# Kernel tuning notes

Hardware: AMD Instinct MI355X
Metric: run time of the kernel (lower is better)

The kernel has to match this reference:

```python
import jax, jax.numpy as jnp
import numpy as np

S, B, H, NH = 2048, 1, 4096, 32
HD = H // NH            # 128
ROT = int(HD * 0.25)    # 32 partial rotary dims
BASE = 10000.0


def setup_inputs() -> dict:
    key = jax.random.key(0)
    ks = jax.random.split(key, 4)
    hidden_states = jax.random.normal(ks[0], (S, B, H), dtype=jnp.float32)
    W_qkv = jax.random.normal(ks[1], (3 * H, H), dtype=jnp.float32) * 0.02
    b_qkv = jnp.zeros((3 * H,), dtype=jnp.float32)
    W_dense = jax.random.normal(ks[2], (H, H), dtype=jnp.float32) * 0.02
    b_dense = jnp.zeros((H,), dtype=jnp.float32)
    # causal left-to-right mask, True = attend
    attention_mask = jnp.tril(jnp.ones((S, S), dtype=bool))[None, None]  # [1,1,S,S]
    return dict(hidden_states=hidden_states, attention_mask=attention_mask,
                W_qkv=W_qkv, b_qkv=b_qkv, W_dense=W_dense, b_dense=b_dense)


def _rotate_half(x):
    x1, x2 = jnp.split(x, 2, axis=-1)
    return jnp.concatenate((-x2, x1), axis=-1)


def reference(hidden_states, attention_mask, W_qkv, b_qkv, W_dense, b_dense):
    S_, B_ = hidden_states.shape[:2]
    qkv = hidden_states @ W_qkv.T + b_qkv                    # [S,B,3H]
    qkv = qkv.reshape(S_, B_, NH, 3 * HD)
    q, k, v = qkv[..., :HD], qkv[..., HD:2 * HD], qkv[..., 2 * HD:]

    # partial rotary embedding (GPT-NeoX style, offset=0, no KV cache)
    inv_freq = 1.0 / (BASE ** (jnp.arange(0, ROT, 2, dtype=jnp.float32) / ROT))
    t = jnp.arange(S_, dtype=jnp.float32)
    freqs = jnp.einsum('s,d->sd', t, inv_freq)               # [S,ROT/2]
    emb = jnp.concatenate((freqs, freqs), axis=-1)           # [S,ROT]
    cos = jnp.cos(emb)[:, None, None, :]                     # [S,1,1,ROT]
    sin = jnp.sin(emb)[:, None, None, :]

    def rope(x):
        return x * cos + _rotate_half(x) * sin

    q = jnp.concatenate((rope(q[..., :ROT]), q[..., ROT:]), axis=-1)
    k = jnp.concatenate((rope(k[..., :ROT]), k[..., ROT:]), axis=-1)

    # scaled dot-product attention with explicit score matrix
    scores = jnp.einsum('sbhd,tbhd->bhst', q, k) / np.float32(np.sqrt(HD))
    scores = jnp.where(attention_mask, scores, jnp.float32(-10000.0))
    probs = jax.nn.softmax(scores, axis=-1)                  # [B,NH,S,S]
    ctx = jnp.einsum('bhst,tbhd->sbhd', probs, v).reshape(S_, B_, H)
    return ctx @ W_dense.T + b_dense                         # [S,B,H]
```

## Files before the change

### kernel.cpp

```cpp
#include <hip/hip_runtime.h>
#include <hip/hip_bf16.h>
#include <math.h>

typedef __bf16 bf16_t;
typedef bf16_t bf16x8 __attribute__((ext_vector_type(8)));
typedef bf16_t bf16x4 __attribute__((ext_vector_type(4)));
typedef float floatx4 __attribute__((ext_vector_type(4)));

#define S_LEN 2048
#define QK_LD 8192

__global__ void convert_all(const float* __restrict__ a, bf16_t* __restrict__ ao,
                            const float* __restrict__ b, bf16_t* __restrict__ bo,
                            const float* __restrict__ c, bf16_t* __restrict__ co) {
    int i = blockIdx.x * 256 + threadIdx.x;
    const float* src; bf16_t* dst; int j;
    if (i < 2097152)        { src = a; dst = ao; j = i; }
    else if (i < 14680064)  { src = b; dst = bo; j = i - 2097152; }
    else                    { src = c; dst = co; j = i - 14680064; }
    float4 v = ((const float4*)src)[j];
    bf16x4 o;
    o.x = (bf16_t)v.x; o.y = (bf16_t)v.y; o.z = (bf16_t)v.z; o.w = (bf16_t)v.w;
    ((bf16x4*)dst)[j] = o;
}

__device__ __forceinline__ void async_copy16(const void* g, void* l) {
    __builtin_amdgcn_global_load_lds(
        (const __attribute__((address_space(1))) unsigned int*)g,
        (__attribute__((address_space(3))) unsigned int*)l, 16, 0, 0);
}

__device__ __forceinline__ void fast_sincos(float x, float* sn, float* cs) {
    float rev = x * 0.15915494309189535f;
    rev = rev - floorf(rev);
    *sn = __builtin_amdgcn_sinf(rev);
    *cs = __builtin_amdgcn_cosf(rev);
}

__global__ __launch_bounds__(256) void qkv_gemm(
    const bf16_t* __restrict__ A, const bf16_t* __restrict__ B,
    const float* __restrict__ bias, bf16_t* __restrict__ qkout,
    bf16_t* __restrict__ vt)
{
    __shared__ bf16_t As[128 * 32];
    __shared__ bf16_t Bs[128 * 32];
    const int K = 4096;
    const int t    = threadIdx.x;
    const int lane = t & 63;
    const int w    = t >> 6;
    const int l15  = lane & 15;
    const int quad = lane >> 4;
    const int bm = blockIdx.y, bn = blockIdx.x;
    const int mw = (w >> 1) * 64, nw = (w & 1) * 64;

    floatx4 acc[4][4];
    #pragma unroll
    for (int i = 0; i < 4; i++)
        #pragma unroll
        for (int j = 0; j < 4; j++)
            acc[i][j] = (floatx4){0.f, 0.f, 0.f, 0.f};

    const int r0 = t >> 2;
    const int c0 = (t & 3) * 8;
    const bf16_t* Aptr = A + (size_t)(bm * 128 + r0) * K + c0;
    const bf16_t* Bptr = B + (size_t)(bn * 128 + r0) * K + c0;
    bf16_t* AsW = As + t * 8;
    bf16_t* BsW = Bs + t * 8;

    for (int k0 = 0; k0 < K; k0 += 32) {
        __syncthreads();
        async_copy16(Aptr + k0, AsW);
        async_copy16(Aptr + k0 + (size_t)64 * K, AsW + 2048);
        async_copy16(Bptr + k0, BsW);
        async_copy16(Bptr + k0 + (size_t)64 * K, BsW + 2048);
        __syncthreads();

        bf16x8 a[4], b[4];
        #pragma unroll
        for (int mi = 0; mi < 4; mi++)
            a[mi] = *(const bf16x8*)&As[(mw + mi * 16 + l15) * 32 + quad * 8];
        #pragma unroll
        for (int ni = 0; ni < 4; ni++)
            b[ni] = *(const bf16x8*)&Bs[(nw + ni * 16 + l15) * 32 + quad * 8];
        #pragma unroll
        for (int mi = 0; mi < 4; mi++)
            #pragma unroll
            for (int ni = 0; ni < 4; ni++)
                acc[mi][ni] = __builtin_amdgcn_mfma_f32_16x16x32_bf16(a[mi], b[ni], acc[mi][ni], 0, 0, 0);
    }

    #pragma unroll
    for (int ni = 0; ni < 4; ni++) {
        float bv = bias[bn * 128 + nw + ni * 16 + l15];
        #pragma unroll
        for (int mi = 0; mi < 4; mi++)
            #pragma unroll
            for (int r = 0; r < 4; r++)
                acc[mi][ni][r] += bv;
    }

    const int h = bn / 3, ht = bn - h * 3;
    if (ht < 2) {
        bf16_t* base = qkout + h * 256 + ht * 128;
        #pragma unroll
        for (int mi = 0; mi < 4; mi++)
            #pragma unroll
            for (int ni = 0; ni < 4; ni++) {
                int col = nw + ni * 16 + l15;
                #pragma unroll
                for (int r = 0; r < 4; r++) {
                    int row = bm * 128 + mw + mi * 16 + quad * 4 + r;
                    base[(size_t)row * QK_LD + col] = (bf16_t)acc[mi][ni][r];
                }
            }
    } else {
        bf16_t* vbase = vt + (size_t)h * 128 * S_LEN;
        #pragma unroll
        for (int mi = 0; mi < 4; mi++) {
            int s0 = bm * 128 + mw + mi * 16 + quad * 4;
            #pragma unroll
            for (int ni = 0; ni < 4; ni++) {
                int d = nw + ni * 16 + l15;
                bf16x4 pv;
                #pragma unroll
                for (int r = 0; r < 4; r++) pv[r] = (bf16_t)acc[mi][ni][r];
                *(bf16x4*)&vbase[(size_t)d * S_LEN + s0] = pv;
            }
        }
    }
}

__global__ void rope_kernel(bf16_t* __restrict__ qk) {
    int idx = blockIdx.x * 256 + threadIdx.x;
    int j = idx & 15;
    int h = (idx >> 4) & 31;
    int s = idx >> 9;
    float invf = exp2f(-(float)j * 0.8304820237218405f);
    float sn, cs;
    fast_sincos((float)s * invf, &sn, &cs);
    bf16_t* base = qk + (size_t)s * QK_LD + h * 256;
    {
        float x1 = (float)base[j], x2 = (float)base[j + 16];
        base[j]      = (bf16_t)(x1 * cs - x2 * sn);
        base[j + 16] = (bf16_t)(x2 * cs + x1 * sn);
    }
    {
        bf16_t* kb = base + 128;
        float x1 = (float)kb[j], x2 = (float)kb[j + 16];
        kb[j]      = (bf16_t)(x1 * cs - x2 * sn);
        kb[j + 16] = (bf16_t)(x2 * cs + x1 * sn);
    }
}

__global__ __launch_bounds__(256) void dense_gemm(
    const bf16_t* __restrict__ A, const bf16_t* __restrict__ B,
    const float* __restrict__ bias, float* __restrict__ C,
    int M, int N, int K)
{
    __shared__ bf16_t As[64 * 32];
    __shared__ bf16_t Bs[128 * 32];
    const int t    = threadIdx.x;
    const int lane = t & 63;
    const int w    = t >> 6;
    const int l15  = lane & 15;
    const int quad = lane >> 4;
    const int bm = blockIdx.y, bn = blockIdx.x;
    const int mw = (w >> 1) * 32, nw = (w & 1) * 64;

    floatx4 acc[2][4];
    #pragma unroll
    for (int i = 0; i < 2; i++)
        #pragma unroll
        for (int j = 0; j < 4; j++)
            acc[i][j] = (floatx4){0.f, 0.f, 0.f, 0.f};

    const int r0 = t >> 2;
    const int c0 = (t & 3) * 8;
    const bf16_t* Aptr = A + (size_t)(bm * 64 + r0) * K + c0;
    const bf16_t* Bptr = B + (size_t)(bn * 128 + r0) * K + c0;
    bf16_t* AsW = As + t * 8;
    bf16_t* BsW = Bs + t * 8;

    for (int k0 = 0; k0 < K; k0 += 32) {
        __syncthreads();
        async_copy16(Aptr + k0, AsW);
        async_copy16(Bptr + k0, BsW);
        async_copy16(Bptr + k0 + (size_t)64 * K, BsW + 2048);
        __syncthreads();

        bf16x8 a[2], b[4];
        #pragma unroll
        for (int mi = 0; mi < 2; mi++)
            a[mi] = *(const bf16x8*)&As[(mw + mi * 16 + l15) * 32 + quad * 8];
        #pragma unroll
        for (int ni = 0; ni < 4; ni++)
            b[ni] = *(const bf16x8*)&Bs[(nw + ni * 16 + l15) * 32 + quad * 8];
        #pragma unroll
        for (int mi = 0; mi < 2; mi++)
            #pragma unroll
            for (int ni = 0; ni < 4; ni++)
                acc[mi][ni] = __builtin_amdgcn_mfma_f32_16x16x32_bf16(a[mi], b[ni], acc[mi][ni], 0, 0, 0);
    }

    #pragma unroll
    for (int ni = 0; ni < 4; ni++) {
        int col = bn * 128 + nw + ni * 16 + l15;
        float bv = bias[col];
        #pragma unroll
        for (int mi = 0; mi < 2; mi++)
            #pragma unroll
            for (int r = 0; r < 4; r++) {
                int row = bm * 64 + mw + mi * 16 + quad * 4 + r;
                C[(size_t)row * N + col] = acc[mi][ni][r] + bv;
            }
    }
}

#define QK_LDS 136
#define V_LDS  72
__global__ __launch_bounds__(256) void flash_attn(
    const bf16_t* __restrict__ qk, const bf16_t* __restrict__ Vt,
    bf16_t* __restrict__ ctx)
{
    __shared__ bf16_t Qs[64 * QK_LDS];
    __shared__ bf16_t Ks[64 * QK_LDS];
    __shared__ bf16_t Vs[128 * V_LDS];
    __shared__ bf16_t Ps[64 * V_LDS];
    const int h = blockIdx.y;
    const int qb = (int)gridDim.x - 1 - blockIdx.x;
    const int t = threadIdx.x;
    const int w = t >> 6, lane = t & 63;
    const int quad = lane >> 4, l15 = lane & 15;
    const float SCL = 0.08838834764831845f * 1.4426950408889634f;

    {
        const bf16_t* qbase = qk + (size_t)(qb * 64) * QK_LD + h * 256;
        int rr = t >> 4, cc = (t & 15) * 8;
        #pragma unroll
        for (int p = 0; p < 4; p++) {
            int row = rr + p * 16;
            *(bf16x8*)&Qs[row * QK_LDS + cc] = *(const bf16x8*)&qbase[(size_t)row * QK_LD + cc];
        }
    }

    floatx4 o[8];
    #pragma unroll
    for (int i = 0; i < 8; i++) o[i] = (floatx4){0.f, 0.f, 0.f, 0.f};
    float lsum[4] = {0.f, 0.f, 0.f, 0.f};

    for (int kt = 0; kt <= qb; kt++) {
        __syncthreads();
        {
            const bf16_t* kbase = qk + (size_t)(kt * 64) * QK_LD + h * 256 + 128;
            int rr = t >> 4, cc = (t & 15) * 8;
            #pragma unroll
            for (int p = 0; p < 4; p++) {
                int row = rr + p * 16;
                *(bf16x8*)&Ks[row * QK_LDS + cc] = *(const bf16x8*)&kbase[(size_t)row * QK_LD + cc];
            }
            const bf16_t* vbase = Vt + (size_t)h * 128 * S_LEN + kt * 64;
            int vr = t >> 3, vc = (t & 7) * 8;
            #pragma unroll
            for (int p = 0; p < 4; p++) {
                int row = vr + p * 32;
                *(bf16x8*)&Vs[row * V_LDS + vc] = *(const bf16x8*)&vbase[(size_t)row * S_LEN + vc];
            }
        }
        __syncthreads();

        floatx4 sacc[4];
        #pragma unroll
        for (int ni = 0; ni < 4; ni++) sacc[ni] = (floatx4){0.f, 0.f, 0.f, 0.f};
        #pragma unroll
        for (int ks = 0; ks < 4; ks++) {
            bf16x8 aq = *(const bf16x8*)&Qs[(w * 16 + l15) * QK_LDS + ks * 32 + quad * 8];
            #pragma unroll
            for (int ni = 0; ni < 4; ni++) {
                bf16x8 bk = *(const bf16x8*)&Ks[(ni * 16 + l15) * QK_LDS + ks * 32 + quad * 8];
                sacc[ni] = __builtin_amdgcn_mfma_f32_16x16x32_bf16(aq, bk, sacc[ni], 0, 0, 0);
            }
        }

        float pv[4][4];
        #pragma unroll
        for (int ni = 0; ni < 4; ni++)
            #pragma unroll
            for (int r = 0; r < 4; r++)
                pv[ni][r] = __builtin_amdgcn_exp2f(sacc[ni][r] * SCL);
        if (kt == qb) {
            #pragma unroll
            for (int ni = 0; ni < 4; ni++) {
                int key = ni * 16 + l15;
                #pragma unroll
                for (int r = 0; r < 4; r++)
                    if (key > w * 16 + quad * 4 + r) pv[ni][r] = 0.f;
            }
        }
        #pragma unroll
        for (int ni = 0; ni < 4; ni++)
            #pragma unroll
            for (int r = 0; r < 4; r++) {
                lsum[r] += pv[ni][r];
                Ps[(w * 16 + quad * 4 + r) * V_LDS + ni * 16 + l15] = (bf16_t)pv[ni][r];
            }
        asm volatile("s_waitcnt lgkmcnt(0)" ::: "memory");

        #pragma unroll
        for (int ks = 0; ks < 2; ks++) {
            bf16x8 ap = *(const bf16x8*)&Ps[(w * 16 + l15) * V_LDS + ks * 32 + quad * 8];
            #pragma unroll
            for (int ni = 0; ni < 8; ni++) {
                bf16x8 bv = *(const bf16x8*)&Vs[(ni * 16 + l15) * V_LDS + ks * 32 + quad * 8];
                o[ni] = __builtin_amdgcn_mfma_f32_16x16x32_bf16(ap, bv, o[ni], 0, 0, 0);
            }
        }
    }

    float invl[4];
    #pragma unroll
    for (int r = 0; r < 4; r++) {
        float s = lsum[r];
        #pragma unroll
        for (int off = 1; off < 16; off <<= 1)
            s += __shfl_xor(s, off, 16);
        invl[r] = 1.f / s;
    }
    bf16_t* cbase = ctx + (size_t)(qb * 64) * 4096 + h * 128;
    #pragma unroll
    for (int ni = 0; ni < 8; ni++) {
        int col = ni * 16 + l15;
        #pragma unroll
        for (int r = 0; r < 4; r++) {
            int row = w * 16 + quad * 4 + r;
            cbase[(size_t)row * 4096 + col] = (bf16_t)(o[ni][r] * invl[r]);
        }
    }
}

extern "C" void kernel_launch(void* const* d_in, const int* in_sizes, int n_in,
                              void* d_out, int out_size, void* d_ws, size_t ws_size,
                              hipStream_t stream) {
    const float* hidden = (const float*)d_in[0];
    const float* Wqkv   = (const float*)d_in[2];
    const float* bqkv   = (const float*)d_in[3];
    const float* Wd     = (const float*)d_in[4];
    const float* bd     = (const float*)d_in[5];
    float* out = (float*)d_out;

    char* ws = (char*)d_ws;
    bf16_t* h_bf    = (bf16_t*)(ws);
    bf16_t* wqkv_bf = (bf16_t*)(ws + 16777216);
    bf16_t* wd_bf   = (bf16_t*)(ws + 117440512);
    bf16_t* qk      = (bf16_t*)(ws + 150994944);
    bf16_t* vt      = (bf16_t*)(ws + 184549376);
    bf16_t* ctx     = (bf16_t*)(ws + 201326592);

    convert_all<<<73728, 256, 0, stream>>>(hidden, h_bf, Wqkv, wqkv_bf, Wd, wd_bf);
    qkv_gemm<<<dim3(96, 16), 256, 0, stream>>>(h_bf, wqkv_bf, bqkv, qk, vt);
    rope_kernel<<<4096, 256, 0, stream>>>(qk);
    flash_attn<<<dim3(32, 32), 256, 0, stream>>>(qk, vt, ctx);
    dense_gemm<<<dim3(32, 32), 256, 0, stream>>>(ctx, wd_bf, bd, out, 2048, 4096, 4096);
}
```

Before: 819.5 us.

## Rewrite QKV GEMM with 256x256 tiles, multi-stage async LDS pipeline, swizzle

Replaces the 128x128 single-buffered QKV GEMM with a 512-thread 256x256 tile kernel. It uses a double-buffered, split-K-half async global-to-LDS pipeline with explicit waitcnt and barrier phasing, an XOR-swizzled LDS layout to avoid bank conflicts, and s_setprio around the MFMA bursts. The goal is to hide global load latency behind MFMAs and to raise arithmetic intensity per block. The cost is heavy register use from a 32-accumulator tile, 128KB of LDS per block, fragile hand-tuned vmcnt accounting, and only 384 blocks to spread across the CUs.

```diff
diff --git a/kernel.cpp b/kernel.cpp
--- a/kernel.cpp
+++ b/kernel.cpp
@@ -37,94 +37,170 @@
     *cs = __builtin_amdgcn_cosf(rev);
 }
 
-__global__ __launch_bounds__(256) void qkv_gemm(
+__global__ __launch_bounds__(512, 2) void qkv_gemm256(
     const bf16_t* __restrict__ A, const bf16_t* __restrict__ B,
     const float* __restrict__ bias, bf16_t* __restrict__ qkout,
     bf16_t* __restrict__ vt)
 {
-    __shared__ bf16_t As[128 * 32];
-    __shared__ bf16_t Bs[128 * 32];
-    const int K = 4096;
-    const int t    = threadIdx.x;
+    __shared__ bf16_t lds[65536];
+    const int t = threadIdx.x;
     const int lane = t & 63;
-    const int w    = t >> 6;
-    const int l15  = lane & 15;
-    const int quad = lane >> 4;
-    const int bm = blockIdx.y, bn = blockIdx.x;
-    const int mw = (w >> 1) * 64, nw = (w & 1) * 64;
-
-    floatx4 acc[4][4];
-    #pragma unroll
-    for (int i = 0; i < 4; i++)
+    const int w = t >> 6;
+    const int l15 = lane & 15, quad = lane >> 4;
+    const int wr = w >> 2, wc = w & 3;
+    const int bm = blockIdx.x & 7, bn = blockIdx.x >> 3;
+
+    const int srow = t >> 2;
+    const int kslot8 = ((t & 3) ^ ((t >> 3) & 3)) << 3;
+    const bf16_t* Ag = A + (size_t)(bm * 256 + srow) * 4096 + kslot8;
+    const bf16_t* Bg = B + (size_t)(bn * 256 + srow) * 4096 + kslot8;
+    bf16_t* ldsW = lds + t * 8;
+
+    const int xorv8 = (quad ^ ((l15 >> 1) & 3)) << 3;
+    const bf16_t* pA0 = lds + (wr * 128 + l15) * 32 + xorv8;
+    const bf16_t* pB0 = lds + 32768 + (wc * 64 + l15) * 32 + xorv8;
+
+    floatx4 acc[8][4];
+    #pragma unroll
+    for (int i = 0; i < 8; i++)
         #pragma unroll
         for (int j = 0; j < 4; j++)
             acc[i][j] = (floatx4){0.f, 0.f, 0.f, 0.f};
 
-    const int r0 = t >> 2;
-    const int c0 = (t & 3) * 8;
-    const bf16_t* Aptr = A + (size_t)(bm * 128 + r0) * K + c0;
-    const bf16_t* Bptr = B + (size_t)(bn * 128 + r0) * K + c0;
-    bf16_t* AsW = As + t * 8;
-    bf16_t* BsW = Bs + t * 8;
-
-    for (int k0 = 0; k0 < K; k0 += 32) {
-        __syncthreads();
-        async_copy16(Aptr + k0, AsW);
-        async_copy16(Aptr + k0 + (size_t)64 * K, AsW + 2048);
-        async_copy16(Bptr + k0, BsW);
-        async_copy16(Bptr + k0 + (size_t)64 * K, BsW + 2048);
-        __syncthreads();
-
-        bf16x8 a[4], b[4];
-        #pragma unroll
-        for (int mi = 0; mi < 4; mi++)
-            a[mi] = *(const bf16x8*)&As[(mw + mi * 16 + l15) * 32 + quad * 8];
-        #pragma unroll
-        for (int ni = 0; ni < 4; ni++)
-            b[ni] = *(const bf16x8*)&Bs[(nw + ni * 16 + l15) * 32 + quad * 8];
-        #pragma unroll
-        for (int mi = 0; mi < 4; mi++)
-            #pragma unroll
-            for (int ni = 0; ni < 4; ni++)
-                acc[mi][ni] = __builtin_amdgcn_mfma_f32_16x16x32_bf16(a[mi], b[ni], acc[mi][ni], 0, 0, 0);
-    }
-
+    bf16x8 a[4], b[4];
+
+#define STAGE_A(tile, kh, dd) do { \
+    const bf16_t* g_ = Ag + (tile) * 64 + (kh) * 32; \
+    bf16_t* l_ = ldsW + ((dd) * 2 + (kh)) * 8192; \
+    async_copy16(g_, l_); \
+    async_copy16(g_ + (size_t)128 * 4096, l_ + 4096); \
+} while (0)
+#define STAGE_B(tile, kh, dd) do { \
+    const bf16_t* g_ = Bg + (tile) * 64 + (kh) * 32; \
+    bf16_t* l_ = ldsW + 32768 + ((dd) * 2 + (kh)) * 8192; \
+    async_copy16(g_, l_); \
+    async_copy16(g_ + (size_t)128 * 4096, l_ + 4096); \
+} while (0)
+#define LOAD_B4(dd, kh) do { \
+    const bf16_t* pb_ = pB0 + ((dd) * 2 + (kh)) * 8192; \
+    b[0] = *(const bf16x8*)(pb_ + 0 * 512); \
+    b[1] = *(const bf16x8*)(pb_ + 1 * 512); \
+    b[2] = *(const bf16x8*)(pb_ + 2 * 512); \
+    b[3] = *(const bf16x8*)(pb_ + 3 * 512); \
+} while (0)
+#define LOAD_A4(dd, kh, ph) do { \
+    const bf16_t* pa_ = pA0 + ((dd) * 2 + (kh)) * 8192 + (ph) * 2048; \
+    a[0] = *(const bf16x8*)(pa_ + 0 * 512); \
+    a[1] = *(const bf16x8*)(pa_ + 1 * 512); \
+    a[2] = *(const bf16x8*)(pa_ + 2 * 512); \
+    a[3] = *(const bf16x8*)(pa_ + 3 * 512); \
+} while (0)
+#define MFMA16(ph) do { \
+    __builtin_amdgcn_s_setprio(1); \
+    _Pragma("unroll") \
+    for (int mi_ = 0; mi_ < 4; mi_++) \
+        _Pragma("unroll") \
+        for (int ni_ = 0; ni_ < 4; ni_++) \
+            acc[(ph) * 4 + mi_][ni_] = __builtin_amdgcn_mfma_f32_16x16x32_bf16( \
+                a[mi_], b[ni_], acc[(ph) * 4 + mi_][ni_], 0, 0, 0); \
+    __builtin_amdgcn_s_setprio(0); \
+} while (0)
+#define PH_MID() do { \
+    __builtin_amdgcn_sched_barrier(0); \
+    __builtin_amdgcn_s_barrier(); \
+    asm volatile("s_waitcnt lgkmcnt(0)" ::: "memory"); \
+    __builtin_amdgcn_sched_barrier(0); \
+} while (0)
+#define PH_END() do { \
+    __builtin_amdgcn_sched_barrier(0); \
+    asm volatile("" ::: "memory"); \
+    __builtin_amdgcn_s_barrier(); \
+} while (0)
+
+    STAGE_A(0, 0, 0); STAGE_B(0, 0, 0);
+    STAGE_A(0, 1, 0); STAGE_B(0, 1, 0);
+    STAGE_A(1, 0, 1); STAGE_B(1, 0, 1);
+    asm volatile("s_waitcnt vmcnt(8)" ::: "memory");
+    __builtin_amdgcn_s_barrier();
+
+    for (int tt = 0; tt < 64; tt += 2) {
+        LOAD_B4(0, 0); LOAD_A4(0, 0, 0);
+        STAGE_A(tt + 1, 1, 1);
+        PH_MID(); MFMA16(0); PH_END();
+
+        LOAD_A4(0, 0, 1);
+        STAGE_B(tt + 1, 1, 1);
+        PH_MID(); MFMA16(1);
+        asm volatile("s_waitcnt vmcnt(8)" ::: "memory");
+        PH_END();
+
+        LOAD_B4(0, 1); LOAD_A4(0, 1, 0);
+        if (tt + 2 < 64) STAGE_A(tt + 2, 0, 0);
+        PH_MID(); MFMA16(0); PH_END();
+
+        LOAD_A4(0, 1, 1);
+        if (tt + 2 < 64) STAGE_B(tt + 2, 0, 0);
+        PH_MID(); MFMA16(1);
+        if (tt + 2 < 64) { asm volatile("s_waitcnt vmcnt(8)" ::: "memory"); }
+        else             { asm volatile("s_waitcnt vmcnt(4)" ::: "memory"); }
+        PH_END();
+
+        LOAD_B4(1, 0); LOAD_A4(1, 0, 0);
+        if (tt + 2 < 64) STAGE_A(tt + 2, 1, 0);
+        PH_MID(); MFMA16(0); PH_END();
+
+        LOAD_A4(1, 0, 1);
+        if (tt + 2 < 64) STAGE_B(tt + 2, 1, 0);
+        PH_MID(); MFMA16(1);
+        if (tt + 2 < 64) { asm volatile("s_waitcnt vmcnt(8)" ::: "memory"); }
+        else             { asm volatile("s_waitcnt vmcnt(0)" ::: "memory"); }
+        PH_END();
+
+        LOAD_B4(1, 1); LOAD_A4(1, 1, 0);
+        if (tt + 3 < 64) STAGE_A(tt + 3, 0, 1);
+        PH_MID(); MFMA16(0); PH_END();
+
+        LOAD_A4(1, 1, 1);
+        if (tt + 3 < 64) STAGE_B(tt + 3, 0, 1);
+        PH_MID(); MFMA16(1);
+        if (tt + 3 < 64) { asm volatile("s_waitcnt vmcnt(8)" ::: "memory"); }
+        PH_END();
+    }
+
+#undef STAGE_A
+#undef STAGE_B
+#undef LOAD_B4
+#undef LOAD_A4
+#undef MFMA16
+#undef PH_MID
+#undef PH_END
+
+    const int colbase = bn * 256 + wc * 64;
     #pragma unroll
     for (int ni = 0; ni < 4; ni++) {
-        float bv = bias[bn * 128 + nw + ni * 16 + l15];
-        #pragma unroll
-        for (int mi = 0; mi < 4; mi++)
-            #pragma unroll
-            for (int r = 0; r < 4; r++)
-                acc[mi][ni][r] += bv;
-    }
-
-    const int h = bn / 3, ht = bn - h * 3;
-    if (ht < 2) {
-        bf16_t* base = qkout + h * 256 + ht * 128;
-        #pragma unroll
-        for (int mi = 0; mi < 4; mi++)
-            #pragma unroll
-            for (int ni = 0; ni < 4; ni++) {
-                int col = nw + ni * 16 + l15;
+        const int cb = colbase + ni * 16;
+        const float bv = bias[cb + l15];
+        const int h = cb / 384;
+        const int rem = cb - h * 384;
+        if (rem < 256) {
+            bf16_t* qb = qkout + (size_t)h * 256 + rem + l15;
+            #pragma unroll
+            for (int mi = 0; mi < 8; mi++) {
+                const int row0 = bm * 256 + wr * 128 + mi * 16 + quad * 4;
                 #pragma unroll
-                for (int r = 0; r < 4; r++) {
-                    int row = bm * 128 + mw + mi * 16 + quad * 4 + r;
-                    base[(size_t)row * QK_LD + col] = (bf16_t)acc[mi][ni][r];
-                }
-            }
-    } else {
-        bf16_t* vbase = vt + (size_t)h * 128 * S_LEN;
-        #pragma unroll
-        for (int mi = 0; mi < 4; mi++) {
-            int s0 = bm * 128 + mw + mi * 16 + quad * 4;
-            #pragma unroll
-            for (int ni = 0; ni < 4; ni++) {
-                int d = nw + ni * 16 + l15;
+                for (int r = 0; r < 4; r++)
+                    qb[(size_t)(row0 + r) * QK_LD] = (bf16_t)(acc[mi][ni][r] + bv);
+            }
+        } else {
+            const int d0 = rem - 256 + l15;
+            bf16_t* vb = vt + ((size_t)h * 128 + d0) * S_LEN;
+            #pragma unroll
+            for (int mi = 0; mi < 8; mi++) {
+                const int row0 = bm * 256 + wr * 128 + mi * 16 + quad * 4;
                 bf16x4 pv;
                 #pragma unroll
-                for (int r = 0; r < 4; r++) pv[r] = (bf16_t)acc[mi][ni][r];
-                *(bf16x4*)&vbase[(size_t)d * S_LEN + s0] = pv;
+                for (int r = 0; r < 4; r++) pv[r] = (bf16_t)(acc[mi][ni][r] + bv);
+                *(bf16x4*)&vb[row0] = pv;
             }
         }
     }
@@ -356,7 +432,7 @@
     bf16_t* ctx     = (bf16_t*)(ws + 201326592);
 
     convert_all<<<73728, 256, 0, stream>>>(hidden, h_bf, Wqkv, wqkv_bf, Wd, wd_bf);
-    qkv_gemm<<<dim3(96, 16), 256, 0, stream>>>(h_bf, wqkv_bf, bqkv, qk, vt);
+    qkv_gemm256<<<dim3(384), 512, 0, stream>>>(h_bf, wqkv_bf, bqkv, qk, vt);
     rope_kernel<<<4096, 256, 0, stream>>>(qk);
     flash_attn<<<dim3(32, 32), 256, 0, stream>>>(qk, vt, ctx);
     dense_gemm<<<dim3(32, 32), 256, 0, stream>>>(ctx, wd_bf, bd, out, 2048, 4096, 4096);
```

Result: no change. 817.1 us (-0.3%).
